# Optimization experiments

Measured on AMD Instinct MI355X. Metric: run time of the kernel, lower is better.

The kernel has to match this reference:

```python
import jax, jax.numpy as jnp
import numpy as np

B = 65536; T = 7
N_NUM = 32; N_CAT = 16; CARD = 100; D_CAT = 16
D_STATE = 96; D_HID = 192; S_DIM = 64; DT = 1.0
D_IN = N_NUM + N_CAT * D_CAT + 8  # 296
D_Z = 3 * D_STATE + 64            # 352

def _ln(x, g, b, eps=1e-5):
    m = x.mean(-1, keepdims=True)
    v = ((x - m) ** 2).mean(-1, keepdims=True)
    return (x - m) * jax.lax.rsqrt(v + eps) * g + b

def _gelu(x):
    return jax.nn.gelu(x, approximate=False)  # matches torch F.gelu default (erf)

def _forward(x_num, x_static, cat_emb, day_emb, xproj_w, xproj_b, h0,
             bln_g, bln_b, fc1_w, fc1_b, fc2_w, fc2_b,
             spln_g, spln_b, sp1_w, sp1_b, sp2_w, sp2_b,
             base_w, base_b, hln_g, hln_b,
             hm1_w, hm1_b, hm2_w, hm2_b,
             hq1_w, hq1_b, hq2_w, hq2_b,
             hn1_w, hn1_b, hn2_w, hn2_b, x_cat):
    Bsz = x_num.shape[0]
    # categorical embeddings: per-feature table lookup -> (B,T,N_CAT,D_CAT)
    emb = jax.vmap(lambda tab, idx: tab[idx], in_axes=(0, 2), out_axes=2)(cat_emb, x_cat)
    emb = emb.reshape(Bsz, T, N_CAT * D_CAT)
    # day ids are arange(1,8), shared over batch
    day = jnp.broadcast_to(day_emb[1:8], (Bsz, T, 8))
    x = jnp.concatenate([x_num, emb, day], axis=-1)          # (B,T,D_IN)
    x = x @ xproj_w + xproj_b                                # (B,T,D_STATE)

    def step(h, xt):  # Euler-integrated LN+MLP residual cell (dropout = eval identity)
        z = jnp.concatenate([h, xt], axis=-1)                # (B,2*D_STATE)
        z = _ln(z, bln_g, bln_b)
        dh = _gelu(z @ fc1_w + fc1_b) @ fc2_w + fc2_b
        h = h + DT * dh
        return h, h

    h0b = jnp.broadcast_to(h0, (Bsz, D_STATE))
    _, hs = jax.lax.scan(step, h0b, jnp.swapaxes(x, 0, 1))   # (T,B,D_STATE)
    H = jnp.swapaxes(hs, 0, 1)                               # (B,T,D_STATE)
    h_last = H[:, -1]
    h_mean = H.mean(axis=1)
    h_max = H.max(axis=1)

    s = _ln(x_static, spln_g, spln_b)
    s64 = _gelu(s @ sp1_w + sp1_b) @ sp2_w + sp2_b           # (B,64)

    z = jnp.concatenate([h_last, h_mean, h_max, s64], axis=-1)  # (B,D_Z)
    z = _ln(z, hln_g, hln_b)
    base = x_static @ base_w + base_b                        # (B,)
    mean = base + _gelu(z @ hm1_w + hm1_b) @ hm2_w + hm2_b
    q20 = base + _gelu(z @ hq1_w + hq1_b) @ hq2_w + hq2_b
    neg_logit = _gelu(z @ hn1_w + hn1_b) @ hn2_w + hn2_b
    return mean, q20, neg_logit

def setup_inputs() -> dict:
    key = jax.random.key(0)
    ks = iter(jax.random.split(key, 64))
    def w(shape, scale=0.02):
        return (scale * jax.random.normal(next(ks), shape)).astype(jnp.float32)
    def zz(shape):
        return jnp.zeros(shape, jnp.float32)
    def oo(shape):
        return jnp.ones(shape, jnp.float32)
    inp = {
        "x_num": jax.random.normal(next(ks), (B, T, N_NUM), jnp.float32),
        "x_static": jax.random.normal(next(ks), (B, S_DIM), jnp.float32),
        "x_cat": jax.random.randint(next(ks), (B, T, N_CAT), 0, CARD),
        "cat_emb": w((N_CAT, CARD + 1, D_CAT), 1.0),
        "day_emb": w((8, 8), 1.0),
        "xproj_w": w((D_IN, D_STATE)), "xproj_b": zz((D_STATE,)),
        "h0": zz((D_STATE,)),
        "bln_g": oo((2 * D_STATE,)), "bln_b": zz((2 * D_STATE,)),
        "fc1_w": w((2 * D_STATE, D_HID)), "fc1_b": zz((D_HID,)),
        "fc2_w": w((D_HID, D_STATE)), "fc2_b": zz((D_STATE,)),
        "spln_g": oo((S_DIM,)), "spln_b": zz((S_DIM,)),
        "sp1_w": w((S_DIM, 128)), "sp1_b": zz((128,)),
        "sp2_w": w((128, 64)), "sp2_b": zz((64,)),
        "base_w": w((S_DIM,)), "base_b": zz(()),
        "hln_g": oo((D_Z,)), "hln_b": zz((D_Z,)),
        "hm1_w": w((D_Z, D_HID)), "hm1_b": zz((D_HID,)),
        "hm2_w": w((D_HID,)), "hm2_b": zz(()),
        "hq1_w": w((D_Z, D_HID)), "hq1_b": zz((D_HID,)),
        "hq2_w": w((D_HID,)), "hq2_b": zz(()),
        "hn1_w": w((D_Z, D_HID // 2)), "hn1_b": zz((D_HID // 2,)),
        "hn2_w": w((D_HID // 2,)), "hn2_b": zz(()),
    }
    return inp

def reference(x_num, x_static, x_cat, cat_emb, day_emb, xproj_w, xproj_b, h0,
              bln_g, bln_b, fc1_w, fc1_b, fc2_w, fc2_b,
              spln_g, spln_b, sp1_w, sp1_b, sp2_w, sp2_b,
              base_w, base_b, hln_g, hln_b,
              hm1_w, hm1_b, hm2_w, hm2_b,
              hq1_w, hq1_b, hq2_w, hq2_b,
              hn1_w, hn1_b, hn2_w, hn2_b):
    return _forward(x_num, x_static, cat_emb, day_emb, xproj_w, xproj_b, h0,
                    bln_g, bln_b, fc1_w, fc1_b, fc2_w, fc2_b,
                    spln_g, spln_b, sp1_w, sp1_b, sp2_w, sp2_b,
                    base_w, base_b, hln_g, hln_b,
                    hm1_w, hm1_b, hm2_w, hm2_b,
                    hq1_w, hq1_b, hq2_w, hq2_b,
                    hn1_w, hn1_b, hn2_w, hn2_b, x_cat)
```

## Files before the change

kernel.cpp:

```cpp
#include <hip/hip_runtime.h>
#include <math.h>

#define NB 65536

typedef __attribute__((ext_vector_type(8))) short bf16x8;
typedef __attribute__((ext_vector_type(4))) float f32x4;

#define O_BIAST  0
#define O_FC1C   4096
#define O_FC1BP  8192
#define O_FC1FR  12288
#define O_FC2FR  86016
#define O_HDFR   122880
#define O_HDC    460800
#define O_HDBP   462848
#define O_W2C    464896
#define O_SPC    466944
#define O_SPB    467968
#define O_SP1FR  468992
#define O_SP2FR  485376
#define O_XP2FR  501760
#define O_EMB16  557056
#define O_FEAT   608768
#define O_S64    38357504
#define O_STAT   46746112
#define O_BASE   47270400
#define O_XROW   47532544
#define O_XSTAT  135612928

__device__ __forceinline__ unsigned short f2b(float x) {
  unsigned int u = __float_as_uint(x);
  u += 0x7fffu + ((u >> 16) & 1u);
  return (unsigned short)(u >> 16);
}
__device__ __forceinline__ float b2f(unsigned short u) {
  return __uint_as_float(((unsigned)u) << 16);
}
__device__ __forceinline__ float geluf(float x) {
  return 0.5f * x * (1.0f + erff(x * 0.70710678118654752f));
}

__global__ void k0_pre(
    const float* __restrict__ cat_emb, const float* __restrict__ day_emb,
    const float* __restrict__ xproj_w, const float* __restrict__ xproj_b,
    const float* __restrict__ bln_g, const float* __restrict__ bln_b,
    const float* __restrict__ fc1_w, const float* __restrict__ fc1_b,
    const float* __restrict__ fc2_w,
    const float* __restrict__ spln_g, const float* __restrict__ spln_b,
    const float* __restrict__ sp1_w, const float* __restrict__ sp1_b,
    const float* __restrict__ sp2_w,
    const float* __restrict__ hln_g, const float* __restrict__ hln_b,
    const float* __restrict__ hm1_w, const float* __restrict__ hm1_b,
    const float* __restrict__ hq1_w, const float* __restrict__ hq1_b,
    const float* __restrict__ hn1_w, const float* __restrict__ hn1_b,
    const float* __restrict__ hm2_w, const float* __restrict__ hq2_w,
    const float* __restrict__ hn2_w,
    char* __restrict__ wsb)
{
  const int b = blockIdx.x, tid = threadIdx.x;
  if (b < 7) {
    if (tid < 96) {
      int t = b;
      float acc = xproj_b[tid];
      #pragma unroll
      for (int d = 0; d < 8; ++d)
        acc = fmaf(day_emb[(1+t)*8 + d], xproj_w[(288+d)*96 + tid], acc);
      ((float*)(wsb + O_BIAST))[t*96 + tid] = acc;
    }
  } else if (b < 9) {
    if (tid < 96) {
      int col = (b-7)*96 + tid;
      float C = 0.f, Bp = fc1_b[col];
      for (int k = 0; k < 192; ++k) {
        float w = fc1_w[k*192 + col];
        C = fmaf(bln_g[k], w, C);
        Bp = fmaf(bln_b[k], w, Bp);
      }
      ((float*)(wsb + O_FC1C))[col] = C;
      ((float*)(wsb + O_FC1BP))[col] = Bp;
    }
  } else if (b < 81) {
    int seg = b - 9, nt = seg / 6, ks = seg - nt*6;
    int ln = tid >> 3, j = tid & 7;
    int k = ks*32 + (ln>>4)*8 + j, col = nt*16 + (ln&15);
    ((unsigned short*)(wsb + O_FC1FR))[(seg*64 + ln)*8 + j] = f2b(bln_g[k]*fc1_w[k*192 + col]);
  } else if (b < 117) {
    int seg = b - 81, nt = seg / 6, ks = seg - nt*6;
    int ln = tid >> 3, j = tid & 7;
    int k = ks*32 + (ln>>4)*8 + j, col = nt*16 + (ln&15);
    ((unsigned short*)(wsb + O_FC2FR))[(seg*64 + ln)*8 + j] = f2b(fc2_w[k*96 + col]);
  } else if (b < 447) {
    int seg = b - 117, nt = seg / 11, ks = seg - nt*11;
    int ln = tid >> 3, j = tid & 7;
    int k = ks*32 + (ln>>4)*8 + j, gcol = nt*16 + (ln&15);
    float w;
    if (gcol < 192) w = hm1_w[k*192 + gcol];
    else if (gcol < 384) w = hq1_w[k*192 + (gcol-192)];
    else w = hn1_w[k*96 + (gcol-384)];
    ((unsigned short*)(wsb + O_HDFR))[(seg*64 + ln)*8 + j] = f2b(hln_g[k]*w);
  } else if (b < 448) {
    if (tid < 480) {
      int gcol = tid;
      float C = 0.f, Bp, w2;
      if (gcol < 192) { Bp = hm1_b[gcol]; w2 = hm2_w[gcol]; }
      else if (gcol < 384) { Bp = hq1_b[gcol-192]; w2 = hq2_w[gcol-192]; }
      else { Bp = hn1_b[gcol-384]; w2 = hn2_w[gcol-384]; }
      for (int k = 0; k < 352; ++k) {
        float w;
        if (gcol < 192) w = hm1_w[k*192 + gcol];
        else if (gcol < 384) w = hq1_w[k*192 + (gcol-192)];
        else w = hn1_w[k*96 + (gcol-384)];
        C = fmaf(hln_g[k], w, C);
        Bp = fmaf(hln_b[k], w, Bp);
      }
      ((float*)(wsb + O_HDC))[gcol] = C;
      ((float*)(wsb + O_HDBP))[gcol] = Bp;
      ((float*)(wsb + O_W2C))[gcol] = w2;
    }
  } else if (b < 449) {
    if (tid < 128) {
      int col = tid;
      float C = 0.f, Bp = sp1_b[col];
      for (int k = 0; k < 64; ++k) {
        float w = sp1_w[k*128 + col];
        C += b2f(f2b(spln_g[k]*w));
        Bp = fmaf(spln_b[k], w, Bp);
      }
      ((float*)(wsb + O_SPC))[col] = C;
      ((float*)(wsb + O_SPB))[col] = Bp;
    }
  } else if (b < 465) {
    int seg = b - 449;
    int ln = tid >> 3, j = tid & 7;
    int nt = seg >> 1, ks = seg & 1;
    int k = ks*32 + (ln>>4)*8 + j, col = nt*16 + (ln&15);
    ((unsigned short*)(wsb + O_SP1FR))[(seg*64 + ln)*8 + j] = f2b(spln_g[k]*sp1_w[k*128 + col]);
  } else if (b < 481) {
    int seg = b - 465;
    int ln = tid >> 3, j = tid & 7;
    int ks = seg & 3;
    int k = ks*32 + (ln>>4)*8 + j, col = (seg >> 2)*16 + (ln&15);
    ((unsigned short*)(wsb + O_SP2FR))[(seg*64 + ln)*8 + j] = f2b(sp2_w[k*64 + col]);
  } else if (b < 535) {
    int seg = b - 481, ks = seg / 6, nt = seg - ks*6;
    int ln = tid >> 3, j = tid & 7;
    int k = ks*32 + (ln>>4)*8 + j, col = nt*16 + (ln&15);
    ((unsigned short*)(wsb + O_XP2FR))[(seg*64 + ln)*8 + j] = f2b(xproj_w[k*96 + col]);
  } else {
    int i = (b - 535)*512 + tid;
    if (i < 25856)
      ((unsigned short*)(wsb + O_EMB16))[i] = f2b(cat_emb[i]);
  }
}

__global__ __launch_bounds__(256) void k1a_xproj(
    const float* __restrict__ x_num, const int* __restrict__ x_cat,
    const char* __restrict__ wsb, unsigned short* __restrict__ xrow,
    float* __restrict__ xstat)
{
  __shared__ float ctile[4][16][100];
  __shared__ float bsh[7][96];
  const int tid = threadIdx.x;
  const int wv = tid >> 6, l = tid & 63, lr = l & 15, lq = l >> 4;
  const unsigned ct = blockIdx.x*64u + wv*16u + lr;
  const int lqh = lq >> 1, lql = lq & 1;

  if (tid < 168)
    ((float4*)bsh)[tid] = ((const float4*)(wsb + O_BIAST))[tid];
  __syncthreads();

  int e0,e1,e2,e3,e4,e5,e6,e7;
  {
    const int4* ip = (const int4*)(x_cat + (size_t)ct*16);
    int4 v0 = ip[0], v1 = ip[1], v2 = ip[2], v3 = ip[3];
    e0 = lqh ? v0.y : v0.x;  e1 = lqh ? v0.w : v0.z;
    e2 = lqh ? v1.y : v1.x;  e3 = lqh ? v1.w : v1.z;
    e4 = lqh ? v2.y : v2.x;  e5 = lqh ? v2.w : v2.z;
    e6 = lqh ? v3.y : v3.x;  e7 = lqh ? v3.w : v3.z;
  }
  const unsigned short* emb = (const unsigned short*)(wsb + O_EMB16);
  bf16x8 af[9];
  {
    const float* xnp = x_num + (size_t)ct*32 + lq*8;
    float xf[8];
    *(float4*)&xf[0] = *(const float4*)xnp;
    *(float4*)&xf[4] = *(const float4*)(xnp + 4);
    union { bf16x8 v; unsigned short u[8]; } au;
    #pragma unroll
    for (int j = 0; j < 8; ++j) au.u[j] = f2b(xf[j]);
    af[0] = au.v;
  }
  af[1] = *(const bf16x8*)(emb + ((0*2+lqh)*101 + e0)*16 + lql*8);
  af[2] = *(const bf16x8*)(emb + ((1*2+lqh)*101 + e1)*16 + lql*8);
  af[3] = *(const bf16x8*)(emb + ((2*2+lqh)*101 + e2)*16 + lql*8);
  af[4] = *(const bf16x8*)(emb + ((3*2+lqh)*101 + e3)*16 + lql*8);
  af[5] = *(const bf16x8*)(emb + ((4*2+lqh)*101 + e4)*16 + lql*8);
  af[6] = *(const bf16x8*)(emb + ((5*2+lqh)*101 + e5)*16 + lql*8);
  af[7] = *(const bf16x8*)(emb + ((6*2+lqh)*101 + e6)*16 + lql*8);
  af[8] = *(const bf16x8*)(emb + ((7*2+lqh)*101 + e7)*16 + lql*8);

  const bf16x8* xp2 = (const bf16x8*)(wsb + O_XP2FR);
  const f32x4 zero4 = {0.f, 0.f, 0.f, 0.f};
  f32x4 acc[6];
  #pragma unroll
  for (int nt = 0; nt < 6; ++nt) acc[nt] = zero4;
  #pragma unroll
  for (int ks = 0; ks < 9; ++ks) {
    #pragma unroll
    for (int nt = 0; nt < 6; ++nt)
      acc[nt] = __builtin_amdgcn_mfma_f32_16x16x32_bf16(af[ks], xp2[(ks*6+nt)*64 + l], acc[nt], 0, 0, 0);
  }
  #pragma unroll
  for (int nt = 0; nt < 6; ++nt) {
    #pragma unroll
    for (int i = 0; i < 4; ++i)
      ctile[wv][lq*4 + i][nt*16 + lr] = acc[nt][i];
  }
  asm volatile("s_waitcnt lgkmcnt(0)" ::: "memory");
  __builtin_amdgcn_sched_barrier(0);
  const unsigned t = ct % 7u;
  float cv[24], bv[24];
  #pragma unroll
  for (int q = 0; q < 6; ++q) {
    *(float4*)&cv[q*4] = *(const float4*)&ctile[wv][lr][lq*24 + q*4];
    *(float4*)&bv[q*4] = *(const float4*)&bsh[t][lq*24 + q*4];
  }
  unsigned ow[12];
  float sm = 0.f, sq = 0.f;
  #pragma unroll
  for (int u = 0; u < 12; ++u) {
    unsigned short u0 = f2b(cv[2*u]   + bv[2*u]);
    unsigned short u1 = f2b(cv[2*u+1] + bv[2*u+1]);
    ow[u] = (unsigned)u0 | ((unsigned)u1 << 16);
    float f0 = b2f(u0), f1 = b2f(u1);
    sm += f0 + f1; sq = fmaf(f0, f0, fmaf(f1, f1, sq));
  }
  {
    uint4* xo = (uint4*)(xrow + (size_t)ct*96 + lq*24);
    xo[0] = make_uint4(ow[0], ow[1], ow[2], ow[3]);
    xo[1] = make_uint4(ow[4], ow[5], ow[6], ow[7]);
    xo[2] = make_uint4(ow[8], ow[9], ow[10], ow[11]);
  }
  sm += __shfl_xor(sm, 16, 64); sm += __shfl_xor(sm, 32, 64);
  sq += __shfl_xor(sq, 16, 64); sq += __shfl_xor(sq, 32, 64);
  if (lq == 0) {
    float2 o; o.x = sm; o.y = sq;
    *(float2*)(xstat + (size_t)ct*2) = o;
  }
}

__global__ __launch_bounds__(512, 2) void k1_scan(
    const float* __restrict__ h0, const float* __restrict__ fc2_b,
    const char* __restrict__ wsb, const unsigned short* __restrict__ xrow,
    const float* __restrict__ xstat, unsigned short* __restrict__ feat,
    float* __restrict__ statg)
{
  extern __shared__ char smem[];
  unsigned short* zg = (unsigned short*)smem;
  unsigned short* f1f = (unsigned short*)(smem + 51200);
  unsigned short* f2f = (unsigned short*)(smem + 124928);

  const int tid = threadIdx.x;
  const int wv = tid >> 6;
  const int l = tid & 63;
  const int lr = l & 15;
  const int lq = l >> 4;
  const int rowt = wv*16 + lr;

  {
    const uint4* s1 = (const uint4*)(wsb + O_FC1FR);
    uint4* d1 = (uint4*)f1f;
    for (int o = tid; o < 4608; o += 512) d1[o] = s1[o];
    const uint4* s2 = (const uint4*)(wsb + O_FC2FR);
    uint4* d2 = (uint4*)f2f;
    for (int o = tid; o < 2304; o += 512) d2[o] = s2[o];
  }
  const bf16x8* f1v = (const bf16x8*)f1f;
  const bf16x8* f2v = (const bf16x8*)f2f;

  float C1[12], B1[12];
  {
    const float* fc1C = (const float*)(wsb + O_FC1C);
    const float* fc1BP = (const float*)(wsb + O_FC1BP);
    #pragma unroll
    for (int nt = 0; nt < 12; ++nt) { C1[nt] = fc1C[nt*16+lr]; B1[nt] = fc1BP[nt*16+lr]; }
  }
  float fb2[6];
  #pragma unroll
  for (int nt = 0; nt < 6; ++nt) fb2[nt] = fc2_b[nt*16+lr];

  float h[24], hs[24], hm[24];
  #pragma unroll
  for (int nt = 0; nt < 6; ++nt) {
    float v = h0[nt*16+lr];
    #pragma unroll
    for (int i = 0; i < 4; ++i) { h[nt*4+i] = v; hs[nt*4+i] = 0.f; hm[nt*4+i] = -3.4e38f; }
  }
  __syncthreads();

  const f32x4 zero4 = {0.f, 0.f, 0.f, 0.f};
  const size_t srow_q = (size_t)blockIdx.x*128 + wv*16;

  for (int t = 0; t < 7; ++t) {
    float hsm[4] = {0.f,0.f,0.f,0.f}, hsq[4] = {0.f,0.f,0.f,0.f};
    #pragma unroll
    for (int nt = 0; nt < 6; ++nt) {
      #pragma unroll
      for (int i = 0; i < 4; ++i) {
        unsigned short hb = f2b(h[nt*4+i]);
        zg[(wv*16 + lq*4 + i)*200 + nt*16 + lr] = hb;
        float hf = b2f(hb);
        hsm[i] += hf; hsq[i] = fmaf(hf, hf, hsq[i]);
      }
    }
    #pragma unroll
    for (int i = 0; i < 4; ++i) {
      hsm[i] += __shfl_xor(hsm[i], 1, 64); hsm[i] += __shfl_xor(hsm[i], 2, 64);
      hsm[i] += __shfl_xor(hsm[i], 4, 64); hsm[i] += __shfl_xor(hsm[i], 8, 64);
      hsq[i] += __shfl_xor(hsq[i], 1, 64); hsq[i] += __shfl_xor(hsq[i], 2, 64);
      hsq[i] += __shfl_xor(hsq[i], 4, 64); hsq[i] += __shfl_xor(hsq[i], 8, 64);
    }
    float mr[4], rr[4];
    #pragma unroll
    for (int i = 0; i < 4; ++i) {
      const float2 xs = *(const float2*)(xstat + ((srow_q + lq*4 + i)*7 + t)*2);
      float m = (hsm[i] + xs.x) * (1.f/192.f);
      float var = (hsq[i] + xs.y) * (1.f/192.f) - m*m;
      mr[i] = m; rr[i] = rsqrtf(var + 1e-5f);
    }
    bf16x8 ax[3];
    {
      const unsigned short* xp = xrow + ((srow_q + lr)*7 + t)*96;
      #pragma unroll
      for (int k3 = 0; k3 < 3; ++k3)
        ax[k3] = *(const bf16x8*)(xp + k3*32 + lq*8);
    }
    f32x4 acc[12];
    #pragma unroll
    for (int nt = 0; nt < 12; ++nt) acc[nt] = zero4;
    #pragma unroll
    for (int ks = 0; ks < 3; ++ks) {
      bf16x8 a = *(const bf16x8*)(zg + rowt*200 + ks*32 + lq*8);
      #pragma unroll
      for (int nt = 0; nt < 12; ++nt)
        acc[nt] = __builtin_amdgcn_mfma_f32_16x16x32_bf16(a, f1v[(nt*6+ks)*64 + l], acc[nt], 0, 0, 0);
    }
    #pragma unroll
    for (int k3 = 0; k3 < 3; ++k3) {
      #pragma unroll
      for (int nt = 0; nt < 12; ++nt)
        acc[nt] = __builtin_amdgcn_mfma_f32_16x16x32_bf16(ax[k3], f1v[(nt*6+k3+3)*64 + l], acc[nt], 0, 0, 0);
    }
    #pragma unroll
    for (int nt = 0; nt < 12; ++nt) {
      #pragma unroll
      for (int i = 0; i < 4; ++i) {
        float hid = rr[i]*(acc[nt][i] - mr[i]*C1[nt]) + B1[nt];
        zg[(wv*16 + lq*4 + i)*200 + nt*16 + lr] = f2b(geluf(hid));
      }
    }
    f32x4 a2[6];
    #pragma unroll
    for (int nt = 0; nt < 6; ++nt) a2[nt] = zero4;
    #pragma unroll
    for (int ks = 0; ks < 6; ++ks) {
      bf16x8 a = *(const bf16x8*)(zg + rowt*200 + ks*32 + lq*8);
      #pragma unroll
      for (int nt = 0; nt < 6; ++nt)
        a2[nt] = __builtin_amdgcn_mfma_f32_16x16x32_bf16(a, f2v[(nt*6+ks)*64 + l], a2[nt], 0, 0, 0);
    }
    #pragma unroll
    for (int nt = 0; nt < 6; ++nt) {
      #pragma unroll
      for (int i = 0; i < 4; ++i) {
        int u = nt*4 + i;
        h[u] += a2[nt][i] + fb2[nt];
        hs[u] += h[u];
        hm[u] = fmaxf(hm[u], h[u]);
      }
    }
  }
  float st[4] = {0.f,0.f,0.f,0.f}, qt[4] = {0.f,0.f,0.f,0.f};
  #pragma unroll
  for (int nt = 0; nt < 6; ++nt) {
    #pragma unroll
    for (int i = 0; i < 4; ++i) {
      size_t r = (srow_q + lq*4 + i)*288;
      int c = nt*16 + lr;
      unsigned short b0 = f2b(h[nt*4+i]);
      unsigned short b1 = f2b(hs[nt*4+i]*(1.f/7.f));
      unsigned short b2v = f2b(hm[nt*4+i]);
      feat[r + c] = b0;
      feat[r + 96 + c] = b1;
      feat[r + 192 + c] = b2v;
      float f0 = b2f(b0), f1 = b2f(b1), f2v = b2f(b2v);
      st[i] += f0 + f1 + f2v;
      qt[i] = fmaf(f0, f0, fmaf(f1, f1, fmaf(f2v, f2v, qt[i])));
    }
  }
  #pragma unroll
  for (int i = 0; i < 4; ++i) {
    st[i] += __shfl_xor(st[i], 1, 64); st[i] += __shfl_xor(st[i], 2, 64);
    st[i] += __shfl_xor(st[i], 4, 64); st[i] += __shfl_xor(st[i], 8, 64);
    qt[i] += __shfl_xor(qt[i], 1, 64); qt[i] += __shfl_xor(qt[i], 2, 64);
    qt[i] += __shfl_xor(qt[i], 4, 64); qt[i] += __shfl_xor(qt[i], 8, 64);
  }
  if (lr == 0) {
    #pragma unroll
    for (int i = 0; i < 4; ++i) {
      size_t r = srow_q + lq*4 + i;
      float2 o; o.x = st[i]; o.y = qt[i];
      *(float2*)(statg + r*2) = o;
    }
  }
}

__global__ __launch_bounds__(512, 2) void k1b_static(
    const float* __restrict__ x_static, const float* __restrict__ sp2_b,
    const float* __restrict__ base_w, const float* __restrict__ base_b,
    char* __restrict__ wsb)
{
  __shared__ char smem[68608];
  unsigned short* sp1f = (unsigned short*)smem;
  unsigned short* sp2f = (unsigned short*)(smem + 16384);
  unsigned short* hid  = (unsigned short*)(smem + 32768);

  const int tid = threadIdx.x;
  const int wv = tid >> 6, l = tid & 63, lr = l & 15, lq = l >> 4;
  const int srow = blockIdx.x*128 + wv*16;

  {
    const uint4* s1 = (const uint4*)(wsb + O_SP1FR);
    uint4* d1 = (uint4*)sp1f;
    for (int o = tid; o < 1024; o += 512) d1[o] = s1[o];
    const uint4* s2 = (const uint4*)(wsb + O_SP2FR);
    uint4* d2 = (uint4*)sp2f;
    for (int o = tid; o < 1024; o += 512) d2[o] = s2[o];
  }
  __syncthreads();

  float x0f[8], x1f[8];
  {
    const float* xr = x_static + (size_t)(srow + lr)*64;
    *(float4*)&x0f[0] = *(const float4*)(xr + lq*8);
    *(float4*)&x0f[4] = *(const float4*)(xr + lq*8 + 4);
    *(float4*)&x1f[0] = *(const float4*)(xr + 32 + lq*8);
    *(float4*)&x1f[4] = *(const float4*)(xr + 32 + lq*8 + 4);
  }
  float sm = 0.f, sq = 0.f, bp = 0.f;
  #pragma unroll
  for (int j = 0; j < 8; ++j) {
    sm += x0f[j] + x1f[j];
    sq = fmaf(x0f[j], x0f[j], fmaf(x1f[j], x1f[j], sq));
    bp = fmaf(x0f[j], base_w[lq*8 + j], fmaf(x1f[j], base_w[32 + lq*8 + j], bp));
  }
  sm += __shfl_xor(sm, 16, 64); sm += __shfl_xor(sm, 32, 64);
  sq += __shfl_xor(sq, 16, 64); sq += __shfl_xor(sq, 32, 64);
  bp += __shfl_xor(bp, 16, 64); bp += __shfl_xor(bp, 32, 64);
  if (lq == 0) ((float*)(wsb + O_BASE))[srow + lr] = bp + base_b[0];
  const float ms = sm*(1.f/64.f);
  const float rs = rsqrtf(sq*(1.f/64.f) - ms*ms + 1e-5f);
  float mr[4], rr[4];
  #pragma unroll
  for (int i = 0; i < 4; ++i) {
    mr[i] = __shfl(ms, lq*4 + i, 16);
    rr[i] = __shfl(rs, lq*4 + i, 16);
  }
  union { bf16x8 v; unsigned short u[8]; } ua0, ua1;
  #pragma unroll
  for (int j = 0; j < 8; ++j) { ua0.u[j] = f2b(x0f[j]); ua1.u[j] = f2b(x1f[j]); }

  const f32x4 zero4 = {0.f, 0.f, 0.f, 0.f};
  const bf16x8* f1 = (const bf16x8*)sp1f;
  const bf16x8* f2 = (const bf16x8*)sp2f;
  unsigned short* hw = hid + wv*2176;

  f32x4 acc[8];
  #pragma unroll
  for (int nt = 0; nt < 8; ++nt) acc[nt] = zero4;
  #pragma unroll
  for (int nt = 0; nt < 8; ++nt) {
    acc[nt] = __builtin_amdgcn_mfma_f32_16x16x32_bf16(ua0.v, f1[(nt*2 + 0)*64 + l], acc[nt], 0, 0, 0);
    acc[nt] = __builtin_amdgcn_mfma_f32_16x16x32_bf16(ua1.v, f1[(nt*2 + 1)*64 + l], acc[nt], 0, 0, 0);
  }
  {
    const float* spC = (const float*)(wsb + O_SPC);
    const float* spB = (const float*)(wsb + O_SPB);
    #pragma unroll
    for (int nt = 0; nt < 8; ++nt) {
      float Cv = spC[nt*16 + lr], Bv = spB[nt*16 + lr];
      #pragma unroll
      for (int i = 0; i < 4; ++i) {
        float hv = rr[i]*(acc[nt][i] - mr[i]*Cv) + Bv;
        hw[(lq*4 + i)*136 + nt*16 + lr] = f2b(geluf(hv));
      }
    }
  }
  f32x4 a2[4];
  #pragma unroll
  for (int nt = 0; nt < 4; ++nt) a2[nt] = zero4;
  #pragma unroll
  for (int ks = 0; ks < 4; ++ks) {
    bf16x8 a = *(const bf16x8*)(hw + lr*136 + ks*32 + lq*8);
    #pragma unroll
    for (int nt = 0; nt < 4; ++nt)
      a2[nt] = __builtin_amdgcn_mfma_f32_16x16x32_bf16(a, f2[(nt*4 + ks)*64 + l], a2[nt], 0, 0, 0);
  }
  float ss[4] = {0.f,0.f,0.f,0.f}, qq[4] = {0.f,0.f,0.f,0.f};
  {
    unsigned short* s64p = (unsigned short*)(wsb + O_S64);
    #pragma unroll
    for (int nt = 0; nt < 4; ++nt) {
      float bv = sp2_b[nt*16 + lr];
      #pragma unroll
      for (int i = 0; i < 4; ++i) {
        unsigned short rb = f2b(a2[nt][i] + bv);
        s64p[(size_t)(srow + lq*4 + i)*64 + nt*16 + lr] = rb;
        float f = b2f(rb);
        ss[i] += f; qq[i] = fmaf(f, f, qq[i]);
      }
    }
  }
  #pragma unroll
  for (int i = 0; i < 4; ++i) {
    ss[i] += __shfl_xor(ss[i], 1, 64); ss[i] += __shfl_xor(ss[i], 2, 64);
    ss[i] += __shfl_xor(ss[i], 4, 64); ss[i] += __shfl_xor(ss[i], 8, 64);
    qq[i] += __shfl_xor(qq[i], 1, 64); qq[i] += __shfl_xor(qq[i], 2, 64);
    qq[i] += __shfl_xor(qq[i], 4, 64); qq[i] += __shfl_xor(qq[i], 8, 64);
  }
  if (lr == 0) {
    float* stat = (float*)(wsb + O_STAT);
    #pragma unroll
    for (int i = 0; i < 4; ++i) {
      size_t r = (size_t)srow + lq*4 + i;
      float2 fs = *(float2*)(stat + r*2);
      float stot = fs.x + ss[i], qtot = fs.y + qq[i];
      float m = stot*(1.f/352.f);
      float var = qtot*(1.f/352.f) - m*m;
      float2 o; o.x = m; o.y = rsqrtf(var + 1e-5f);
      *(float2*)(stat + r*2) = o;
    }
  }
}

__global__ __launch_bounds__(512, 2) void k2b_heads(
    const float* __restrict__ hm2_b, const float* __restrict__ hq2_b,
    const float* __restrict__ hn2_b, const char* __restrict__ wsb,
    const unsigned short* __restrict__ feat, float* __restrict__ out)
{
  extern __shared__ char smem[];
  const int g = blockIdx.y;
  const int tid = threadIdx.x;
  const int wv = tid >> 6, l = tid & 63, lr = l & 15, lq = l >> 4;
  const int ntn = (g == 2) ? 6 : 12;
  {
    const uint4* src = (const uint4*)(wsb + O_HDFR + (size_t)g*135168);
    uint4* dst = (uint4*)smem;
    const int n = ntn*11*64;
    for (int o = tid; o < n; o += 512) dst[o] = src[o];
  }
  __syncthreads();
  const bf16x8* wfr = (const bf16x8*)smem;
  const float* hdC = (const float*)(wsb + O_HDC);
  const float* hdB = (const float*)(wsb + O_HDBP);
  const float* w2c = (const float*)(wsb + O_W2C);
  const float* stat = (const float*)(wsb + O_STAT);
  const float* baseb = (const float*)(wsb + O_BASE);
  const unsigned short* s64p = (const unsigned short*)(wsb + O_S64);
  const float hb = (g == 0) ? hm2_b[0] : (g == 1) ? hq2_b[0] : hn2_b[0];
  const f32x4 zero4 = {0.f, 0.f, 0.f, 0.f};

  for (int c = blockIdx.x; c < 256; c += gridDim.x) {
    const int base = c*256 + wv*32;
    bf16x8 afr0[11], afr1[11];
    {
      const unsigned short* fr0 = feat + (size_t)(base + lr)*288;
      const unsigned short* fr1 = feat + (size_t)(base + 16 + lr)*288;
      #pragma unroll
      for (int ks = 0; ks < 9; ++ks) {
        afr0[ks] = *(const bf16x8*)(fr0 + ks*32 + lq*8);
        afr1[ks] = *(const bf16x8*)(fr1 + ks*32 + lq*8);
      }
      const unsigned short* sr0 = s64p + (size_t)(base + lr)*64;
      const unsigned short* sr1 = s64p + (size_t)(base + 16 + lr)*64;
      afr0[9]  = *(const bf16x8*)(sr0 + lq*8);
      afr0[10] = *(const bf16x8*)(sr0 + 32 + lq*8);
      afr1[9]  = *(const bf16x8*)(sr1 + lq*8);
      afr1[10] = *(const bf16x8*)(sr1 + 32 + lq*8);
    }
    float mr0[4], rr0[4], mr1[4], rr1[4];
    #pragma unroll
    for (int i = 0; i < 4; ++i) {
      float2 s0 = *(const float2*)(stat + (size_t)(base + lq*4 + i)*2);
      float2 s1 = *(const float2*)(stat + (size_t)(base + 16 + lq*4 + i)*2);
      mr0[i] = s0.x; rr0[i] = s0.y; mr1[i] = s1.x; rr1[i] = s1.y;
    }
    float pr0[4] = {0.f,0.f,0.f,0.f}, pr1[4] = {0.f,0.f,0.f,0.f};
    for (int nt = 0; nt < ntn; ++nt) {
      const int col = (g*12 + nt)*16 + lr;
      const float Cv = hdC[col], Bv = hdB[col], w2v = w2c[col];
      f32x4 a0 = zero4, a1v = zero4;
      #pragma unroll
      for (int ks = 0; ks < 11; ++ks) {
        bf16x8 b = wfr[(nt*11 + ks)*64 + l];
        a0  = __builtin_amdgcn_mfma_f32_16x16x32_bf16(afr0[ks], b, a0, 0, 0, 0);
        a1v = __builtin_amdgcn_mfma_f32_16x16x32_bf16(afr1[ks], b, a1v, 0, 0, 0);
      }
      #pragma unroll
      for (int i = 0; i < 4; ++i) {
        pr0[i] += geluf(rr0[i]*(a0[i]  - mr0[i]*Cv) + Bv) * w2v;
        pr1[i] += geluf(rr1[i]*(a1v[i] - mr1[i]*Cv) + Bv) * w2v;
      }
    }
    #pragma unroll
    for (int i = 0; i < 4; ++i) {
      float v0 = pr0[i], v1 = pr1[i];
      v0 += __shfl_xor(v0, 1, 64); v0 += __shfl_xor(v0, 2, 64);
      v0 += __shfl_xor(v0, 4, 64); v0 += __shfl_xor(v0, 8, 64);
      v1 += __shfl_xor(v1, 1, 64); v1 += __shfl_xor(v1, 2, 64);
      v1 += __shfl_xor(v1, 4, 64); v1 += __shfl_xor(v1, 8, 64);
      if (lr == 0) {
        int r0 = base + lq*4 + i;
        int r1 = base + 16 + lq*4 + i;
        float b0 = (g < 2) ? baseb[r0] : 0.f;
        float b1 = (g < 2) ? baseb[r1] : 0.f;
        out[(size_t)g*NB + r0] = b0 + hb + v0;
        out[(size_t)g*NB + r1] = b1 + hb + v1;
      }
    }
  }
}

extern "C" void kernel_launch(void* const* d_in, const int* in_sizes, int n_in,
                              void* d_out, int out_size, void* d_ws, size_t ws_size,
                              hipStream_t stream) {
  (void)in_sizes; (void)n_in; (void)out_size; (void)ws_size;
  const float* x_num    = (const float*)d_in[0];
  const float* x_static = (const float*)d_in[1];
  const int*   x_cat    = (const int*)  d_in[2];
  const float* cat_emb  = (const float*)d_in[3];
  const float* day_emb  = (const float*)d_in[4];
  const float* xproj_w  = (const float*)d_in[5];
  const float* xproj_b  = (const float*)d_in[6];
  const float* h0       = (const float*)d_in[7];
  const float* bln_g    = (const float*)d_in[8];
  const float* bln_b    = (const float*)d_in[9];
  const float* fc1_w    = (const float*)d_in[10];
  const float* fc1_b    = (const float*)d_in[11];
  const float* fc2_w    = (const float*)d_in[12];
  const float* fc2_b    = (const float*)d_in[13];
  const float* spln_g   = (const float*)d_in[14];
  const float* spln_b   = (const float*)d_in[15];
  const float* sp1_w    = (const float*)d_in[16];
  const float* sp1_b    = (const float*)d_in[17];
  const float* sp2_w    = (const float*)d_in[18];
  const float* sp2_b    = (const float*)d_in[19];
  const float* base_w   = (const float*)d_in[20];
  const float* base_b   = (const float*)d_in[21];
  const float* hln_g    = (const float*)d_in[22];
  const float* hln_b    = (const float*)d_in[23];
  const float* hm1_w    = (const float*)d_in[24];
  const float* hm1_b    = (const float*)d_in[25];
  const float* hm2_w    = (const float*)d_in[26];
  const float* hm2_b    = (const float*)d_in[27];
  const float* hq1_w    = (const float*)d_in[28];
  const float* hq1_b    = (const float*)d_in[29];
  const float* hq2_w    = (const float*)d_in[30];
  const float* hq2_b    = (const float*)d_in[31];
  const float* hn1_w    = (const float*)d_in[32];
  const float* hn1_b    = (const float*)d_in[33];
  const float* hn2_w    = (const float*)d_in[34];
  const float* hn2_b    = (const float*)d_in[35];

  char* wsb = (char*)d_ws;
  unsigned short* feat = (unsigned short*)(wsb + O_FEAT);
  unsigned short* xrow = (unsigned short*)(wsb + O_XROW);
  float* xstat = (float*)(wsb + O_XSTAT);
  float* statg = (float*)(wsb + O_STAT);
  float* out = (float*)d_out;

  k0_pre<<<586, 512, 0, stream>>>(cat_emb, day_emb, xproj_w, xproj_b,
      bln_g, bln_b, fc1_w, fc1_b, fc2_w, spln_g, spln_b, sp1_w, sp1_b, sp2_w,
      hln_g, hln_b, hm1_w, hm1_b, hq1_w, hq1_b, hn1_w, hn1_b,
      hm2_w, hq2_w, hn2_w, wsb);
  k1a_xproj<<<7168, 256, 0, stream>>>(x_num, x_cat, wsb, xrow, xstat);
  k1_scan<<<512, 512, 161792, stream>>>(h0, fc2_b, wsb, xrow, xstat, feat, statg);
  k1b_static<<<512, 512, 0, stream>>>(x_static, sp2_b, base_w, base_b, wsb);
  k2b_heads<<<dim3(86, 3), 512, 135168, stream>>>(hm2_b, hq2_b, hn2_b,
      wsb, feat, out);
}
```

Measured before the change: 319.4 us.

## Split each scan row tile across two waves by output columns

The scan kernel now launches 1024 threads per block and pairs waves so each pair shares a 16-row tile. Each wave of the pair computes half of the fc1 and fc2 output columns and owns half of the hidden state. LayerNorm partial sums and the final stats are exchanged through shared memory. This adds block-wide barriers each timestep to gain more waves for latency hiding and fewer registers per thread. The 161792-byte dynamic LDS still limits residency to one block per CU, so the launch bound of 4 blocks cannot be reached.

Result: slower. 394.8 us (+23.6%).

```diff
diff --git a/kernel.cpp b/kernel.cpp
--- a/kernel.cpp
+++ b/kernel.cpp
@@ -249,7 +249,7 @@
   }
 }
 
-__global__ __launch_bounds__(512, 2) void k1_scan(
+__global__ __launch_bounds__(1024, 4) void k1_scan(
     const float* __restrict__ h0, const float* __restrict__ fc2_b,
     const char* __restrict__ wsb, const unsigned short* __restrict__ xrow,
     const float* __restrict__ xstat, unsigned short* __restrict__ feat,
@@ -262,53 +262,58 @@
 
   const int tid = threadIdx.x;
   const int wv = tid >> 6;
+  const int pr = wv >> 1;
+  const int sub = wv & 1;
   const int l = tid & 63;
   const int lr = l & 15;
   const int lq = l >> 4;
-  const int rowt = wv*16 + lr;
+  const int rowt = pr*16 + lr;
 
   {
     const uint4* s1 = (const uint4*)(wsb + O_FC1FR);
     uint4* d1 = (uint4*)f1f;
-    for (int o = tid; o < 4608; o += 512) d1[o] = s1[o];
+    for (int o = tid; o < 4608; o += 1024) d1[o] = s1[o];
     const uint4* s2 = (const uint4*)(wsb + O_FC2FR);
     uint4* d2 = (uint4*)f2f;
-    for (int o = tid; o < 2304; o += 512) d2[o] = s2[o];
+    for (int o = tid; o < 2304; o += 1024) d2[o] = s2[o];
   }
   const bf16x8* f1v = (const bf16x8*)f1f;
   const bf16x8* f2v = (const bf16x8*)f2f;
 
-  float C1[12], B1[12];
+  float C1[6], B1[6];
   {
     const float* fc1C = (const float*)(wsb + O_FC1C);
     const float* fc1BP = (const float*)(wsb + O_FC1BP);
     #pragma unroll
-    for (int nt = 0; nt < 12; ++nt) { C1[nt] = fc1C[nt*16+lr]; B1[nt] = fc1BP[nt*16+lr]; }
-  }
-  float fb2[6];
-  #pragma unroll
-  for (int nt = 0; nt < 6; ++nt) fb2[nt] = fc2_b[nt*16+lr];
-
-  float h[24], hs[24], hm[24];
-  #pragma unroll
-  for (int nt = 0; nt < 6; ++nt) {
-    float v = h0[nt*16+lr];
+    for (int nt = 0; nt < 6; ++nt) {
+      C1[nt] = fc1C[(sub*6+nt)*16+lr];
+      B1[nt] = fc1BP[(sub*6+nt)*16+lr];
+    }
+  }
+  float fb2[3];
+  #pragma unroll
+  for (int nt = 0; nt < 3; ++nt) fb2[nt] = fc2_b[(sub*3+nt)*16+lr];
+
+  float h[12], hs[12], hm[12];
+  #pragma unroll
+  for (int nt = 0; nt < 3; ++nt) {
+    float v = h0[(sub*3+nt)*16+lr];
     #pragma unroll
     for (int i = 0; i < 4; ++i) { h[nt*4+i] = v; hs[nt*4+i] = 0.f; hm[nt*4+i] = -3.4e38f; }
   }
   __syncthreads();
 
   const f32x4 zero4 = {0.f, 0.f, 0.f, 0.f};
-  const size_t srow_q = (size_t)blockIdx.x*128 + wv*16;
+  const size_t srow_q = (size_t)blockIdx.x*128 + pr*16;
 
   for (int t = 0; t < 7; ++t) {
     float hsm[4] = {0.f,0.f,0.f,0.f}, hsq[4] = {0.f,0.f,0.f,0.f};
     #pragma unroll
-    for (int nt = 0; nt < 6; ++nt) {
+    for (int nt = 0; nt < 3; ++nt) {
       #pragma unroll
       for (int i = 0; i < 4; ++i) {
         unsigned short hb = f2b(h[nt*4+i]);
-        zg[(wv*16 + lq*4 + i)*200 + nt*16 + lr] = hb;
+        zg[(pr*16 + lq*4 + i)*200 + (sub*3+nt)*16 + lr] = hb;
         float hf = b2f(hb);
         hsm[i] += hf; hsq[i] = fmaf(hf, hf, hsq[i]);
       }
@@ -320,12 +325,23 @@
       hsq[i] += __shfl_xor(hsq[i], 1, 64); hsq[i] += __shfl_xor(hsq[i], 2, 64);
       hsq[i] += __shfl_xor(hsq[i], 4, 64); hsq[i] += __shfl_xor(hsq[i], 8, 64);
     }
+    if (lr == 0) {
+      #pragma unroll
+      for (int i = 0; i < 4; ++i) {
+        float2 v; v.x = hsm[i]; v.y = hsq[i];
+        *(float2*)(zg + (pr*16 + lq*4 + i)*200 + 192 + sub*4) = v;
+      }
+    }
+    __syncthreads();
     float mr[4], rr[4];
     #pragma unroll
     for (int i = 0; i < 4; ++i) {
+      const int r = pr*16 + lq*4 + i;
+      float2 p0 = *(const float2*)(zg + r*200 + 192);
+      float2 p1 = *(const float2*)(zg + r*200 + 196);
       const float2 xs = *(const float2*)(xstat + ((srow_q + lq*4 + i)*7 + t)*2);
-      float m = (hsm[i] + xs.x) * (1.f/192.f);
-      float var = (hsq[i] + xs.y) * (1.f/192.f) - m*m;
+      float m = (p0.x + p1.x + xs.x) * (1.f/192.f);
+      float var = (p0.y + p1.y + xs.y) * (1.f/192.f) - m*m;
       mr[i] = m; rr[i] = rsqrtf(var + 1e-5f);
     }
     bf16x8 ax[3];
@@ -335,42 +351,43 @@
       for (int k3 = 0; k3 < 3; ++k3)
         ax[k3] = *(const bf16x8*)(xp + k3*32 + lq*8);
     }
-    f32x4 acc[12];
-    #pragma unroll
-    for (int nt = 0; nt < 12; ++nt) acc[nt] = zero4;
+    f32x4 acc[6];
+    #pragma unroll
+    for (int nt = 0; nt < 6; ++nt) acc[nt] = zero4;
     #pragma unroll
     for (int ks = 0; ks < 3; ++ks) {
       bf16x8 a = *(const bf16x8*)(zg + rowt*200 + ks*32 + lq*8);
       #pragma unroll
-      for (int nt = 0; nt < 12; ++nt)
-        acc[nt] = __builtin_amdgcn_mfma_f32_16x16x32_bf16(a, f1v[(nt*6+ks)*64 + l], acc[nt], 0, 0, 0);
+      for (int nt = 0; nt < 6; ++nt)
+        acc[nt] = __builtin_amdgcn_mfma_f32_16x16x32_bf16(a, f1v[((sub*6+nt)*6+ks)*64 + l], acc[nt], 0, 0, 0);
     }
     #pragma unroll
     for (int k3 = 0; k3 < 3; ++k3) {
       #pragma unroll
-      for (int nt = 0; nt < 12; ++nt)
-        acc[nt] = __builtin_amdgcn_mfma_f32_16x16x32_bf16(ax[k3], f1v[(nt*6+k3+3)*64 + l], acc[nt], 0, 0, 0);
-    }
-    #pragma unroll
-    for (int nt = 0; nt < 12; ++nt) {
+      for (int nt = 0; nt < 6; ++nt)
+        acc[nt] = __builtin_amdgcn_mfma_f32_16x16x32_bf16(ax[k3], f1v[((sub*6+nt)*6+k3+3)*64 + l], acc[nt], 0, 0, 0);
+    }
+    #pragma unroll
+    for (int nt = 0; nt < 6; ++nt) {
       #pragma unroll
       for (int i = 0; i < 4; ++i) {
         float hid = rr[i]*(acc[nt][i] - mr[i]*C1[nt]) + B1[nt];
-        zg[(wv*16 + lq*4 + i)*200 + nt*16 + lr] = f2b(geluf(hid));
-      }
-    }
-    f32x4 a2[6];
-    #pragma unroll
-    for (int nt = 0; nt < 6; ++nt) a2[nt] = zero4;
+        zg[(pr*16 + lq*4 + i)*200 + sub*96 + nt*16 + lr] = f2b(geluf(hid));
+      }
+    }
+    __syncthreads();
+    f32x4 a2[3];
+    #pragma unroll
+    for (int nt = 0; nt < 3; ++nt) a2[nt] = zero4;
     #pragma unroll
     for (int ks = 0; ks < 6; ++ks) {
       bf16x8 a = *(const bf16x8*)(zg + rowt*200 + ks*32 + lq*8);
       #pragma unroll
-      for (int nt = 0; nt < 6; ++nt)
-        a2[nt] = __builtin_amdgcn_mfma_f32_16x16x32_bf16(a, f2v[(nt*6+ks)*64 + l], a2[nt], 0, 0, 0);
-    }
-    #pragma unroll
-    for (int nt = 0; nt < 6; ++nt) {
+      for (int nt = 0; nt < 3; ++nt)
+        a2[nt] = __builtin_amdgcn_mfma_f32_16x16x32_bf16(a, f2v[((sub*3+nt)*6+ks)*64 + l], a2[nt], 0, 0, 0);
+    }
+    #pragma unroll
+    for (int nt = 0; nt < 3; ++nt) {
       #pragma unroll
       for (int i = 0; i < 4; ++i) {
         int u = nt*4 + i;
@@ -379,14 +396,15 @@
         hm[u] = fmaxf(hm[u], h[u]);
       }
     }
+    __syncthreads();
   }
   float st[4] = {0.f,0.f,0.f,0.f}, qt[4] = {0.f,0.f,0.f,0.f};
   #pragma unroll
-  for (int nt = 0; nt < 6; ++nt) {
+  for (int nt = 0; nt < 3; ++nt) {
     #pragma unroll
     for (int i = 0; i < 4; ++i) {
       size_t r = (srow_q + lq*4 + i)*288;
-      int c = nt*16 + lr;
+      int c = (sub*3+nt)*16 + lr;
       unsigned short b0 = f2b(h[nt*4+i]);
       unsigned short b1 = f2b(hs[nt*4+i]*(1.f/7.f));
       unsigned short b2v = f2b(hm[nt*4+i]);
@@ -408,9 +426,19 @@
   if (lr == 0) {
     #pragma unroll
     for (int i = 0; i < 4; ++i) {
-      size_t r = srow_q + lq*4 + i;
-      float2 o; o.x = st[i]; o.y = qt[i];
-      *(float2*)(statg + r*2) = o;
+      float2 v; v.x = st[i]; v.y = qt[i];
+      *(float2*)(zg + (pr*16 + lq*4 + i)*200 + 192 + sub*4) = v;
+    }
+  }
+  __syncthreads();
+  if (sub == 0 && lr == 0) {
+    #pragma unroll
+    for (int i = 0; i < 4; ++i) {
+      const int r = pr*16 + lq*4 + i;
+      float2 p0 = *(const float2*)(zg + r*200 + 192);
+      float2 p1 = *(const float2*)(zg + r*200 + 196);
+      float2 o; o.x = p0.x + p1.x; o.y = p0.y + p1.y;
+      *(float2*)(statg + (srow_q + lq*4 + i)*2) = o;
     }
   }
 }
@@ -684,7 +712,7 @@
       hln_g, hln_b, hm1_w, hm1_b, hq1_w, hq1_b, hn1_w, hn1_b,
       hm2_w, hq2_w, hn2_w, wsb);
   k1a_xproj<<<7168, 256, 0, stream>>>(x_num, x_cat, wsb, xrow, xstat);
-  k1_scan<<<512, 512, 161792, stream>>>(h0, fc2_b, wsb, xrow, xstat, feat, statg);
+  k1_scan<<<512, 1024, 161792, stream>>>(h0, fc2_b, wsb, xrow, xstat, feat, statg);
   k1b_static<<<512, 512, 0, stream>>>(x_static, sp2_b, base_w, base_b, wsb);
   k2b_heads<<<dim3(86, 3), 512, 135168, stream>>>(hm2_b, hq2_b, hn2_b,
       wsb, feat, out);
```
